# Optimization experiments

Measured on AMD Instinct MI355X. Metric: run time of the kernel, lower is better.

Reference implementation:

```python
import jax, jax.numpy as jnp
import numpy as np

C = 64           # channels
CPG = 8          # channel_per_group
G = C // CPG     # offset groups = 8
K = 27           # 3x3x3 taps
N, D, H, W = 2, 8, 56, 56


def conv3d(x, w, b=None):
    y = jax.lax.conv_general_dilated(
        x, w, window_strides=(1, 1, 1), padding=[(1, 1)] * 3,
        dimension_numbers=('NCDHW', 'OIDHW', 'NCDHW'))
    if b is not None:
        y = y + b.reshape(1, -1, 1, 1, 1)
    return y


def deform_conv3d(x, off, w, groups):
    # x: [N,C,D,H,W]; off: [N, G*3*27, D,H,W]; w: [O,C,3,3,3]
    n, cin, d, h, wd = x.shape
    cpg = cin // groups
    p = d * h * wd
    off = off.reshape(n, groups, K, 3, d, h, wd)
    # kernel tap displacements in (kd,kh,kw) order, each in {-1,0,1}
    r = jnp.arange(3, dtype=x.dtype) - 1.0
    taps = jnp.stack(jnp.meshgrid(r, r, r, indexing='ij'), axis=-1).reshape(K, 3)
    gd = jnp.arange(d, dtype=x.dtype)[:, None, None]
    gh = jnp.arange(h, dtype=x.dtype)[None, :, None]
    gw = jnp.arange(wd, dtype=x.dtype)[None, None, :]
    # sampling positions [N,G,K,D,H,W]
    pd = gd + taps[:, 0][:, None, None, None] + off[:, :, :, 0]
    ph = gh + taps[:, 1][:, None, None, None] + off[:, :, :, 1]
    pw = gw + taps[:, 2][:, None, None, None] + off[:, :, :, 2]
    d0 = jnp.floor(pd); h0 = jnp.floor(ph); w0 = jnp.floor(pw)
    fd, fh, fw = pd - d0, ph - h0, pw - w0
    d0 = d0.astype(jnp.int32); h0 = h0.astype(jnp.int32); w0 = w0.astype(jnp.int32)
    xflat = x.reshape(n, groups, cpg, p)[:, :, None]  # [N,G,1,Cpg,P]
    acc = jnp.zeros((n, groups, K, cpg, p), x.dtype)
    for cd in (0, 1):
        for ch in (0, 1):
            for cw in (0, 1):
                idd, idh, idw = d0 + cd, h0 + ch, w0 + cw
                wgt = ((fd if cd else 1.0 - fd)
                       * (fh if ch else 1.0 - fh)
                       * (fw if cw else 1.0 - fw))
                valid = ((idd >= 0) & (idd < d) & (idh >= 0) & (idh < h)
                         & (idw >= 0) & (idw < wd)).astype(x.dtype)
                lin = ((jnp.clip(idd, 0, d - 1) * h + jnp.clip(idh, 0, h - 1)) * wd
                       + jnp.clip(idw, 0, wd - 1))
                g = jnp.take_along_axis(xflat, lin.reshape(n, groups, K, 1, p), axis=-1)
                acc = acc + g * (wgt * valid).reshape(n, groups, K, 1, p)
    # [N,G,K,Cpg,P] -> [N,K,C,P]
    vals = acc.transpose(0, 2, 1, 3, 4).reshape(n, K, cin, p)
    out = jnp.einsum('oik,nkip->nop', w.reshape(w.shape[0], cin, K), vals)
    return out.reshape(n, -1, d, h, wd)


def batchnorm(x, gamma, beta, eps=1e-5):
    m = x.mean((0, 2, 3, 4), keepdims=True)
    v = x.var((0, 2, 3, 4), keepdims=True)
    return (gamma.reshape(1, -1, 1, 1, 1) * (x - m) * jax.lax.rsqrt(v + eps)
            + beta.reshape(1, -1, 1, 1, 1))


def setup_inputs() -> dict:
    key = jax.random.key(0)
    ks = jax.random.split(key, 4)
    fan = C * K
    x = jax.random.normal(ks[0], (N, C, D, H, W), jnp.float32)
    w_off = jax.random.normal(ks[1], (G * 3 * K, C, 3, 3, 3), jnp.float32) * 0.01
    b_off = jnp.zeros((G * 3 * K,), jnp.float32)
    w1 = jax.random.normal(ks[2], (C, C, 3, 3, 3), jnp.float32) / np.sqrt(fan).astype(np.float32)
    w2 = jax.random.normal(ks[3], (C, C, 3, 3, 3), jnp.float32) / np.sqrt(fan).astype(np.float32)
    return dict(x=x, w_off=w_off, b_off=b_off, w1=w1,
                gamma1=jnp.ones((C,), jnp.float32), beta1=jnp.zeros((C,), jnp.float32),
                w2=w2, b2=jnp.zeros((C,), jnp.float32),
                gamma2=jnp.ones((C,), jnp.float32), beta2=jnp.zeros((C,), jnp.float32))


def reference(x, w_off, b_off, w1, gamma1, beta1, w2, b2, gamma2, beta2):
    residual = x
    off = conv3d(x, w_off, b_off)
    out = deform_conv3d(x, off, w1, G)
    out = jax.nn.relu(batchnorm(out, gamma1, beta1))
    out = conv3d(out, w2, b2)
    out = batchnorm(out, gamma2, beta2) + residual
    return jax.nn.relu(out)
```

## Files before the change

kernel.cpp:

```cpp
#include <hip/hip_runtime.h>
#include <hip/hip_bf16.h>

#define N_ 2
#define C_ 64
#define D_ 8
#define H_ 56
#define W_ 56
#define HW_ (H_*W_)
#define P_ (D_*HW_)
#define G_ 8
#define CPG_ 8
#define K_ 27
#define CO_OFF_ 648
#define MP_ 768
#define KK_ 1728
#define KB_ (KK_*2)

typedef __attribute__((ext_vector_type(8))) short shortx8;
typedef __attribute__((ext_vector_type(4))) float floatx4;
#define AS1 __attribute__((address_space(1)))
#define AS3 __attribute__((address_space(3)))

__device__ inline float b2f(unsigned short u) {
    union { unsigned u; float f; } x; x.u = ((unsigned)u) << 16; return x.f;
}
__device__ inline unsigned short f2b(float f) {
    union { float f; unsigned u; } x; x.f = f;
    unsigned r = (x.u + 0x7fffu + ((x.u >> 16) & 1u)) >> 16;
    return (unsigned short)r;
}
__device__ inline float lof(unsigned u) { union { unsigned u; float f; } x; x.u = u << 16; return x.f; }
__device__ inline float hif(unsigned u) { union { unsigned u; float f; } x; x.u = u & 0xffff0000u; return x.f; }
__device__ inline unsigned cvt_pk_bf16(float a, float b) {
    unsigned r;
    asm("v_cvt_pk_bf16_f32 %0, %1, %2" : "=v"(r) : "v"(a), "v"(b));
    return r;
}


__global__ __launch_bounds__(256) void prep_kernel(
    const float* __restrict__ x,      unsigned short* __restrict__ xt,
    const float* __restrict__ w_off,  unsigned short* __restrict__ A1k,
    const float* __restrict__ w1,     unsigned short* __restrict__ A1t,
    const float* __restrict__ w2,     unsigned short* __restrict__ A2t)
{
    __shared__ unsigned short tile[64][65];
    int b   = blockIdx.x;
    int tid = threadIdx.x;

    if (b < 784) {
        int n  = b / (P_/64);
        int p0 = (b % (P_/64))*64;
        int j  = tid & 63;
        int c0 = (tid >> 6)*16;
        for (int r = 0; r < 16; ++r)
            tile[c0 + r][j] = f2b(x[((size_t)n*C_ + c0 + r)*P_ + p0 + j]);
        __syncthreads();
        unsigned* dst = (unsigned*)(xt + ((size_t)n*P_ + p0)*C_);
        #pragma unroll
        for (int it = 0; it < 8; ++it) {
            int wi  = it*256 + tid;
            int row = wi >> 5;
            int c   = (wi & 31)*2;
            unsigned lo = tile[c][row], hi = tile[c+1][row];
            dst[(size_t)row*32 + (wi & 31)] = lo | (hi << 16);
        }
    } else if (b < 784 + 5184) {
        int i = (b - 784)*256 + tid;
        int m = i / KK_, r = i % KK_;
        int kk = r / 64, ci = r % 64;
        A1k[i] = (m < CO_OFF_) ? f2b(w_off[((size_t)m*C_ + ci)*K_ + kk]) : (unsigned short)0;
    } else if (b < 784 + 5184 + 432) {
        int i = (b - 784 - 5184)*256 + tid;
        int o = i / KK_, r = i % KK_;
        int k = r / 64, ii = r % 64;
        A1t[i] = f2b(w1[((size_t)o*C_ + ii)*K_ + k]);
    } else {
        int i = (b - 784 - 5184 - 432)*256 + tid;
        int o = i / KK_, r = i % KK_;
        int k = r / 64, ii = r % 64;
        A2t[i] = f2b(w2[((size_t)o*C_ + ii)*K_ + k]);
    }
}

__global__ __launch_bounds__(256, 2) void conv_off_fused(
    const unsigned short* __restrict__ A,
    const unsigned short* __restrict__ xt,
    const float* __restrict__ bias,
    unsigned short* __restrict__ off2)
{
    __shared__ __align__(16) short SH[35840];
    int tid = threadIdx.x;
    int w = tid >> 6, lane = tid & 63;
    int lm = lane & 15, lq = lane >> 4;

    if (blockIdx.x < 2*490) {
        short* As0 = SH;
        short* Bs  = SH + 2*16*512;
        int n   = blockIdx.x / 490;
        int bid = blockIdx.x % 490;
        int mt = bid / 98, nt = bid % 98;
        int m0 = mt*128, p0 = nt*256;

        const unsigned short* xtn = xt + (size_t)n*P_*C_;
        unsigned short* out2 = off2 + (size_t)n*216*P_*3;

        const char* Ab0 = (const char*)A + (size_t)(m0 + w*32 + lm)*KB_ + lq*16;
        const char* Ab1 = Ab0 + (size_t)16*KB_;

        int oct = lane & 7;
        int prj[8], dj[8], hj[8], wj[8];
        #pragma unroll
        for (int j = 0; j < 8; ++j) {
            int prow = j*32 + w*8 + (lane >> 3);
            prj[j] = prow;
            int p = p0 + prow;
            dj[j] = p / HW_;
            int hw2 = p % HW_;
            hj[j] = hw2 / W_;
            wj[j] = hw2 % W_;
        }

        auto stageA = [&](int kt, int buf) {
            __builtin_amdgcn_global_load_lds((const AS1 unsigned*)(Ab0 + kt*128),      (AS3 unsigned*)(As0 + buf*8192 + (w*2)*512),     16, 0, 0);
            __builtin_amdgcn_global_load_lds((const AS1 unsigned*)(Ab1 + kt*128),      (AS3 unsigned*)(As0 + buf*8192 + (w*2+1)*512),   16, 0, 0);
            __builtin_amdgcn_global_load_lds((const AS1 unsigned*)(Ab0 + kt*128 + 64), (AS3 unsigned*)(As0 + buf*8192 + (8+w*2)*512),   16, 0, 0);
            __builtin_amdgcn_global_load_lds((const AS1 unsigned*)(Ab1 + kt*128 + 64), (AS3 unsigned*)(As0 + buf*8192 + (8+w*2+1)*512), 16, 0, 0);
        };
        auto loadB = [&](int kt, uint4* B) {
            int kd = kt/9 - 1, kh = (kt/3)%3 - 1, kw = kt%3 - 1;
            int delta = kd*HW_ + kh*W_ + kw;
            #pragma unroll
            for (int j = 0; j < 8; ++j) {
                bool v = ((unsigned)(dj[j]+kd) < (unsigned)D_) &&
                         ((unsigned)(hj[j]+kh) < (unsigned)H_) &&
                         ((unsigned)(wj[j]+kw) < (unsigned)W_);
                uint4 val = {0u,0u,0u,0u};
                if (v) val = *(const uint4*)(xtn + (size_t)(p0 + prj[j] + delta)*C_ + oct*8);
                B[j] = val;
            }
        };

        int mh = w >> 1, nh = w & 1;
        floatx4 acc[4][8];
        #pragma unroll
        for (int i = 0; i < 4; ++i)
            #pragma unroll
            for (int j = 0; j < 8; ++j)
                acc[i][j] = (floatx4){0.f, 0.f, 0.f, 0.f};

        uint4 Bcur[8], Bnext[8];
        #pragma unroll
        for (int j = 0; j < 8; ++j) Bnext[j] = (uint4){0u,0u,0u,0u};
        stageA(0, 0);
        loadB(0, Bcur);

        for (int kt = 0; kt < 27; ++kt) {
            int buf = kt & 1;
            __syncthreads();
            #pragma unroll
            for (int j = 0; j < 8; ++j) {
                int chunk = (oct>>2)*16 + (prj[j]>>4);
                *(uint4*)&Bs[chunk*512 + ((oct&3)*16 + ((prj[j]&15) ^ oct))*8] = Bcur[j];
            }
            __syncthreads();
            if (kt < 26) { stageA(kt+1, buf^1); loadB(kt+1, Bnext); }
            #pragma unroll
            for (int ks = 0; ks < 2; ++ks) {
                int swzB = (lq*16 + (lm ^ (ks*4 + lq)))*8;
                shortx8 a[4];
                #pragma unroll
                for (int i = 0; i < 4; ++i) a[i] = *(const shortx8*)&As0[buf*8192 + (ks*8 + 4*mh + i)*512 + lane*8];
                #pragma unroll
                for (int j = 0; j < 8; ++j) {
                    shortx8 b = *(const shortx8*)&Bs[(ks*16 + 8*nh + j)*512 + swzB];
                    #pragma unroll
                    for (int i = 0; i < 4; ++i)
                        acc[i][j] = __builtin_amdgcn_mfma_f32_16x16x32_bf16(a[i], b, acc[i][j], 0, 0, 0);
                }
            }
            #pragma unroll
            for (int j = 0; j < 8; ++j) Bcur[j] = Bnext[j];
        }

        #pragma unroll
        for (int i = 0; i < 4; ++i) {
            int cob = m0 + (4*mh+i)*16 + lq*4;
            #pragma unroll
            for (int r = 0; r < 4; ++r) {
                int co = cob + r;
                float bv = bias[co];
                int row2 = co / 3, comp = co % 3;
                size_t base = (size_t)row2*P_*3 + comp;
                #pragma unroll
                for (int j = 0; j < 8; ++j) {
                    int col = p0 + (8*nh+j)*16 + lm;
                    out2[base + (size_t)col*3] = f2b(acc[i][j][r] + bv);
                }
            }
        }
    } else {
        short* As = SH;
        short* Bs = SH + 54*512;
        int t  = blockIdx.x - 2*490;
        int n  = t / 196;
        int p0 = (t % 196)*128;

        const unsigned short* xtn = xt + (size_t)n*P_*C_;
        unsigned short* out2 = off2 + (size_t)n*216*P_*3;

        const char* Abase = (const char*)A + (size_t)(640 + lm)*KB_ + lq*16;
        for (int ch = w; ch < 54; ch += 4)
            __builtin_amdgcn_global_load_lds((const AS1 unsigned*)(Abase + ch*64),
                                             (AS3 unsigned*)(As + ch*512), 16, 0, 0);

        int oct = lane & 7;
        int prj[4], dj[4], hj[4], wj[4];
        #pragma unroll
        for (int j = 0; j < 4; ++j) {
            int prow = j*32 + w*8 + (lane >> 3);
            prj[j] = prow;
            int p = p0 + prow;
            dj[j] = p / HW_;
            int hw2 = p % HW_;
            hj[j] = hw2 / W_;
            wj[j] = hw2 % W_;
        }
        auto loadB = [&](int kt, uint4* B) {
            int kd = kt/9 - 1, kh = (kt/3)%3 - 1, kw = kt%3 - 1;
            int delta = kd*HW_ + kh*W_ + kw;
            #pragma unroll
            for (int j = 0; j < 4; ++j) {
                bool v = ((unsigned)(dj[j]+kd) < (unsigned)D_) &&
                         ((unsigned)(hj[j]+kh) < (unsigned)H_) &&
                         ((unsigned)(wj[j]+kw) < (unsigned)W_);
                uint4 val = {0u,0u,0u,0u};
                if (v) val = *(const uint4*)(xtn + (size_t)(p0 + prj[j] + delta)*C_ + oct*8);
                B[j] = val;
            }
        };

        floatx4 acc[2];
        acc[0] = (floatx4){0.f,0.f,0.f,0.f};
        acc[1] = (floatx4){0.f,0.f,0.f,0.f};

        uint4 Bcur[4], Bnext[4];
        #pragma unroll
        for (int j = 0; j < 4; ++j) Bnext[j] = (uint4){0u,0u,0u,0u};
        loadB(0, Bcur);

        for (int kt = 0; kt < 27; ++kt) {
            __syncthreads();
            #pragma unroll
            for (int j = 0; j < 4; ++j) {
                int chunk = (oct>>2)*8 + (prj[j]>>4);
                *(uint4*)&Bs[chunk*512 + ((oct&3)*16 + ((prj[j]&15) ^ oct))*8] = Bcur[j];
            }
            __syncthreads();
            if (kt < 26) loadB(kt+1, Bnext);
            #pragma unroll
            for (int ks = 0; ks < 2; ++ks) {
                int swzB = (lq*16 + (lm ^ (ks*4 + lq)))*8;
                shortx8 a = *(const shortx8*)&As[(kt*2 + ks)*512 + lane*8];
                #pragma unroll
                for (int j = 0; j < 2; ++j) {
                    shortx8 b = *(const shortx8*)&Bs[(ks*8 + w*2 + j)*512 + swzB];
                    acc[j] = __builtin_amdgcn_mfma_f32_16x16x32_bf16(a, b, acc[j], 0, 0, 0);
                }
            }
            #pragma unroll
            for (int j = 0; j < 4; ++j) Bcur[j] = Bnext[j];
        }

        #pragma unroll
        for (int j = 0; j < 2; ++j) {
            #pragma unroll
            for (int r = 0; r < 4; ++r) {
                int co = 640 + lq*4 + r;
                if (co < CO_OFF_) {
                    int col = p0 + w*32 + j*16 + lm;
                    out2[((size_t)(co/3)*P_ + col)*3 + (co%3)] = f2b(acc[j][r] + bias[co]);
                }
            }
        }
    }
}

__global__ __launch_bounds__(256) void deform_fused(
    const unsigned short* __restrict__ xt,
    const unsigned short* __restrict__ off2,
    const unsigned short* __restrict__ A,
    unsigned short* __restrict__ y1t,
    float* __restrict__ bn1p)
{
    __shared__ __align__(16) short SH[12288];
    int tid = threadIdx.x;
    int w = tid >> 6, lane = tid & 63;
    int n  = blockIdx.x / (P_/32);
    int p0 = (blockIdx.x % (P_/32))*32;
    int lm = lane & 15, lq = lane >> 4;

    const unsigned short* offn = off2 + (size_t)n*216*P_*3;
    const uint4* xg0 = (const uint4*)(xt + (size_t)n*P_*C_);

    const char* Ab = (const char*)A + (size_t)(w*16 + lm)*KB_ + lq*16;

    int g = lane & 7;
    int prow = tid >> 3;
    int p = p0 + prow;
    int dd = p / HW_;
    int hw2 = p % HW_;
    int hh = hw2 / W_;
    int ww = hw2 % W_;
    int bchunk = (g>>2)*2 + (prow>>4);
    int boffs  = ((g&3)*16 + ((prow&15) ^ g))*8;

    auto stageA = [&](int kt, int buf) {
        __builtin_amdgcn_global_load_lds((const AS1 unsigned*)(Ab + kt*128),      (AS3 unsigned*)(SH + buf*4096 + w*512),     16, 0, 0);
        __builtin_amdgcn_global_load_lds((const AS1 unsigned*)(Ab + kt*128 + 64), (AS3 unsigned*)(SH + buf*4096 + (4+w)*512), 16, 0, 0);
    };
    auto loadOff = [&](int kt, float* o) {
        size_t idx = ((size_t)(g*K_ + kt)*P_ + p)*3;
        o[0] = b2f(offn[idx]);
        o[1] = b2f(offn[idx + 1]);
        o[2] = b2f(offn[idx + 2]);
    };
    auto issueCorners = [&](int kt, float* o, uint4* V, float* Wt) {
        int kd = kt/9 - 1, kh = (kt/3)%3 - 1, kw = kt%3 - 1;
        float pd = (float)(dd + kd) + o[0];
        float ph = (float)(hh + kh) + o[1];
        float pw = (float)(ww + kw) + o[2];
        float fd0 = floorf(pd), fh0 = floorf(ph), fw0 = floorf(pw);
        int d0 = (int)fd0, h0 = (int)fh0, w0i = (int)fw0;
        float fd = pd - fd0, fh = ph - fh0, fw = pw - fw0;
        int dc0 = min(max(d0, 0), D_-1),   dc1 = min(max(d0+1, 0), D_-1);
        int hc0 = min(max(h0, 0), H_-1),   hc1 = min(max(h0+1, 0), H_-1);
        int wc0 = min(max(w0i, 0), W_-1),  wc1 = min(max(w0i+1, 0), W_-1);
        float wd0 = ((unsigned)d0      < (unsigned)D_) ? 1.f - fd : 0.f;
        float wd1 = ((unsigned)(d0+1)  < (unsigned)D_) ? fd       : 0.f;
        float wh0 = ((unsigned)h0      < (unsigned)H_) ? 1.f - fh : 0.f;
        float wh1 = ((unsigned)(h0+1)  < (unsigned)H_) ? fh       : 0.f;
        float ww0 = ((unsigned)w0i     < (unsigned)W_) ? 1.f - fw : 0.f;
        float ww1 = ((unsigned)(w0i+1) < (unsigned)W_) ? fw       : 0.f;
        int rb00 = (dc0*H_ + hc0)*W_, rb01 = (dc0*H_ + hc1)*W_;
        int rb10 = (dc1*H_ + hc0)*W_, rb11 = (dc1*H_ + hc1)*W_;
        float wdh00 = wd0*wh0, wdh01 = wd0*wh1, wdh10 = wd1*wh0, wdh11 = wd1*wh1;
        V[0] = xg0[(size_t)(rb00+wc0)*8 + g];  Wt[0] = wdh00*ww0;
        V[1] = xg0[(size_t)(rb00+wc1)*8 + g];  Wt[1] = wdh00*ww1;
        V[2] = xg0[(size_t)(rb01+wc0)*8 + g];  Wt[2] = wdh01*ww0;
        V[3] = xg0[(size_t)(rb01+wc1)*8 + g];  Wt[3] = wdh01*ww1;
        V[4] = xg0[(size_t)(rb10+wc0)*8 + g];  Wt[4] = wdh10*ww0;
        V[5] = xg0[(size_t)(rb10+wc1)*8 + g];  Wt[5] = wdh10*ww1;
        V[6] = xg0[(size_t)(rb11+wc0)*8 + g];  Wt[6] = wdh11*ww0;
        V[7] = xg0[(size_t)(rb11+wc1)*8 + g];  Wt[7] = wdh11*ww1;
    };
    auto reduceCorners = [&](uint4* V, float* Wt, uint4& o4) {
        float res[CPG_];
        #pragma unroll
        for (int c = 0; c < CPG_; ++c) res[c] = 0.f;
        #pragma unroll
        for (int c = 0; c < 8; ++c) {
            uint4 v4 = V[c];
            float wgt = Wt[c];
            res[0] = fmaf(wgt, lof(v4.x), res[0]);
            res[1] = fmaf(wgt, hif(v4.x), res[1]);
            res[2] = fmaf(wgt, lof(v4.y), res[2]);
            res[3] = fmaf(wgt, hif(v4.y), res[3]);
            res[4] = fmaf(wgt, lof(v4.z), res[4]);
            res[5] = fmaf(wgt, hif(v4.z), res[5]);
            res[6] = fmaf(wgt, lof(v4.w), res[6]);
            res[7] = fmaf(wgt, hif(v4.w), res[7]);
        }
        o4.x = cvt_pk_bf16(res[0], res[1]);
        o4.y = cvt_pk_bf16(res[2], res[3]);
        o4.z = cvt_pk_bf16(res[4], res[5]);
        o4.w = cvt_pk_bf16(res[6], res[7]);
    };

    int mh = w >> 1, nh = w & 1;
    floatx4 acc[2];
    acc[0] = (floatx4){0.f,0.f,0.f,0.f};
    acc[1] = (floatx4){0.f,0.f,0.f,0.f};

    float offA[3], offB[3], offT[3];
    uint4 Vv[8]; float Wt[8];
    uint4 o4cur;

    stageA(0, 0);
    loadOff(0, offA);
    loadOff(1, offB);
    issueCorners(0, offA, Vv, Wt);
    reduceCorners(Vv, Wt, o4cur);
    *(uint4*)&SH[8192 + bchunk*512 + boffs] = o4cur;

    for (int kt = 0; kt < 27; ++kt) {
        int buf = kt & 1;
        __syncthreads();
        if (kt < 26) {
            stageA(kt+1, buf^1);
            if (kt < 25) loadOff(kt+2, offT);
            issueCorners(kt+1, offB, Vv, Wt);
        }
        #pragma unroll
        for (int ks = 0; ks < 2; ++ks) {
            int swzB = (lq*16 + (lm ^ (ks*4 + lq)))*8;
            shortx8 b = *(const shortx8*)&SH[8192 + buf*2048 + (ks*2 + nh)*512 + swzB];
            #pragma unroll
            for (int i = 0; i < 2; ++i) {
                shortx8 a = *(const shortx8*)&SH[buf*4096 + (ks*4 + 2*mh+i)*512 + lane*8];
                acc[i] = __builtin_amdgcn_mfma_f32_16x16x32_bf16(a, b, acc[i], 0, 0, 0);
            }
        }
        if (kt < 26) {
            reduceCorners(Vv, Wt, o4cur);
            *(uint4*)&SH[8192 + (buf^1)*2048 + bchunk*512 + boffs] = o4cur;
            offB[0] = offT[0]; offB[1] = offT[1]; offB[2] = offT[2];
        }
    }

    __syncthreads();
    #pragma unroll
    for (int i = 0; i < 2; ++i) {
        int ob = mh*32 + i*16 + lq*4;
        int pc = nh*16 + lm;
        #pragma unroll
        for (int rr = 0; rr < 4; ++rr)
            SH[pc*72 + ob + rr] = (short)f2b(acc[i][rr]);
    }
    __syncthreads();
    {
        int row = tid >> 3, seg = tid & 7;
        uint4 v = *(const uint4*)&SH[row*72 + seg*8];
        *(uint4*)(y1t + ((size_t)n*P_ + p0 + row)*C_ + seg*8) = v;
    }
    {
        float* FS = (float*)(SH + 2560);
        float* FQ = FS + 256;
        int o = tid & 63, qt = tid >> 6;
        float s = 0.f, q = 0.f;
        #pragma unroll
        for (int pp = 0; pp < 8; ++pp) {
            float v = b2f((unsigned short)SH[(qt*8 + pp)*72 + o]);
            s += v;
            q = fmaf(v, v, q);
        }
        FS[qt*64 + o] = s;
        FQ[qt*64 + o] = q;
        __syncthreads();
        if (tid < 64) {
            float S = FS[tid] + FS[64+tid] + FS[128+tid] + FS[192+tid];
            float Q = FQ[tid] + FQ[64+tid] + FQ[128+tid] + FQ[192+tid];
            bn1p[(size_t)blockIdx.x*128 + tid]      = S;
            bn1p[(size_t)blockIdx.x*128 + 64 + tid] = Q;
        }
    }
}

__global__ __launch_bounds__(256) void conv2_fused(
    const unsigned short* __restrict__ y1t,
    const float* __restrict__ st1,
    const unsigned short* __restrict__ A,
    const float* __restrict__ bias,
    unsigned short* __restrict__ y2,
    float* __restrict__ part2)
{
    __shared__ __align__(16) short As[4][4096];
    __shared__ float sc[64], sf[64];
    __shared__ float SP[4][64], SQ[4][64];
    int tid = threadIdx.x;
    if (tid < 64) sc[tid] = st1[tid];
    else if (tid < 128) sf[tid-64] = st1[tid];
    int w = tid >> 6, lane = tid & 63;
    int n  = blockIdx.x / (P_/128);
    int p0 = (blockIdx.x % (P_/128))*128;
    int lm = lane & 15, lq = lane >> 4;

    const unsigned short* y1n = y1t + (size_t)n*P_*C_;
    unsigned short* y2n = y2 + (size_t)n*C_*P_;
    const char* Ab = (const char*)A + (size_t)(w*16 + lm)*KB_ + lq*16;

    int pj[2], dd[2], hh[2], ww[2];
    #pragma unroll
    for (int j = 0; j < 2; ++j) {
        pj[j] = p0 + j*64 + w*16 + lm;
        dd[j] = pj[j] / HW_;
        int hw2 = pj[j] % HW_;
        hh[j] = hw2 / W_;
        ww[j] = hw2 % W_;
    }

    auto stageA = [&](int kt) {
        int buf = kt & 3;
        __builtin_amdgcn_global_load_lds((const AS1 unsigned*)(Ab + kt*128),      (AS3 unsigned*)(&As[buf][w*512]),     16, 0, 0);
        __builtin_amdgcn_global_load_lds((const AS1 unsigned*)(Ab + kt*128 + 64), (AS3 unsigned*)(&As[buf][(4+w)*512]), 16, 0, 0);
    };
    auto issueV = [&](int kt, uint4 (*V)[2], int* M) {
        int kd = kt/9 - 1, kh = (kt/3)%3 - 1, kw = kt%3 - 1;
        int delta = kd*HW_ + kh*W_ + kw;
        #pragma unroll
        for (int j = 0; j < 2; ++j) {
            bool v = ((unsigned)(dd[j]+kd) < (unsigned)D_) &&
                     ((unsigned)(hh[j]+kh) < (unsigned)H_) &&
                     ((unsigned)(ww[j]+kw) < (unsigned)W_);
            M[j] = v ? 1 : 0;
            #pragma unroll
            for (int ks = 0; ks < 2; ++ks) {
                uint4 val = {0u,0u,0u,0u};
                if (v) val = *(const uint4*)(y1n + (size_t)(pj[j] + delta)*C_ + (ks*4 + lq)*8);
                V[j][ks] = val;
            }
        }
    };
    auto reduceT = [&](uint4 V, int ks, int M) -> shortx8 {
        uint4 o4 = {0u,0u,0u,0u};
        if (M) {
            int cb = (ks*4 + lq)*8;
            float r0 = fmaxf(lof(V.x)*sc[cb+0] + sf[cb+0], 0.f);
            float r1 = fmaxf(hif(V.x)*sc[cb+1] + sf[cb+1], 0.f);
            float r2 = fmaxf(lof(V.y)*sc[cb+2] + sf[cb+2], 0.f);
            float r3 = fmaxf(hif(V.y)*sc[cb+3] + sf[cb+3], 0.f);
            float r4 = fmaxf(lof(V.z)*sc[cb+4] + sf[cb+4], 0.f);
            float r5 = fmaxf(hif(V.z)*sc[cb+5] + sf[cb+5], 0.f);
            float r6 = fmaxf(lof(V.w)*sc[cb+6] + sf[cb+6], 0.f);
            float r7 = fmaxf(hif(V.w)*sc[cb+7] + sf[cb+7], 0.f);
            o4.x = cvt_pk_bf16(r0, r1);
            o4.y = cvt_pk_bf16(r2, r3);
            o4.z = cvt_pk_bf16(r4, r5);
            o4.w = cvt_pk_bf16(r6, r7);
        }
        return *(shortx8*)&o4;
    };

    floatx4 acc[4][2];
    #pragma unroll
    for (int i = 0; i < 4; ++i)
        #pragma unroll
        for (int j = 0; j < 2; ++j)
            acc[i][j] = (floatx4){0.f,0.f,0.f,0.f};

    auto mfmaTap = [&](int kt, uint4 (*V)[2], const int* M) {
        int buf = kt & 3;
        #pragma unroll
        for (int j = 0; j < 2; ++j) {
            shortx8 b0 = reduceT(V[j][0], 0, M[j]);
            shortx8 b1 = reduceT(V[j][1], 1, M[j]);
            #pragma unroll
            for (int i = 0; i < 4; ++i) {
                shortx8 a = *(const shortx8*)&As[buf][(0*4 + i)*512 + lane*8];
                acc[i][j] = __builtin_amdgcn_mfma_f32_16x16x32_bf16(a, b0, acc[i][j], 0, 0, 0);
            }
            #pragma unroll
            for (int i = 0; i < 4; ++i) {
                shortx8 a = *(const shortx8*)&As[buf][(1*4 + i)*512 + lane*8];
                acc[i][j] = __builtin_amdgcn_mfma_f32_16x16x32_bf16(a, b1, acc[i][j], 0, 0, 0);
            }
        }
    };

    uint4 VA[2][2], VB[2][2];
    int MA[2], MB[2];
    stageA(0); stageA(1);
    issueV(0, VA, MA);
    issueV(1, VB, MB);

    for (int kt = 0; kt < 26; kt += 2) {
        __syncthreads();
        stageA(kt+2);
        if (kt+3 <= 26) stageA(kt+3);
        {
            uint4 Vc[2][2];
            #pragma unroll
            for (int j = 0; j < 2; ++j) { Vc[j][0] = VA[j][0]; Vc[j][1] = VA[j][1]; }
            int Mc[2] = {MA[0], MA[1]};
            issueV(kt+2, VA, MA);
            mfmaTap(kt, Vc, Mc);
        }
        {
            uint4 Vc[2][2];
            #pragma unroll
            for (int j = 0; j < 2; ++j) { Vc[j][0] = VB[j][0]; Vc[j][1] = VB[j][1]; }
            int Mc[2] = {MB[0], MB[1]};
            if (kt+3 <= 26) issueV(kt+3, VB, MB);
            mfmaTap(kt+1, Vc, Mc);
        }
    }
    __syncthreads();
    mfmaTap(26, VA, MA);

    #pragma unroll
    for (int i = 0; i < 4; ++i) {
        #pragma unroll
        for (int r = 0; r < 4; ++r) {
            int co = i*16 + lq*4 + r;
            float v0 = acc[i][0][r] + bias[co];
            float v1 = acc[i][1][r] + bias[co];
            y2n[(size_t)co*P_ + pj[0]] = f2b(v0);
            y2n[(size_t)co*P_ + pj[1]] = f2b(v1);
            float s = v0 + v1;
            float q = v0*v0 + v1*v1;
            #pragma unroll
            for (int m = 1; m < 16; m <<= 1) {
                s += __shfl_xor(s, m);
                q += __shfl_xor(q, m);
            }
            if (lm == 0) { SP[w][co] = s; SQ[w][co] = q; }
        }
    }
    __syncthreads();
    if (tid < 64) {
        float S = SP[0][tid] + SP[1][tid] + SP[2][tid] + SP[3][tid];
        float Q = SQ[0][tid] + SQ[1][tid] + SQ[2][tid] + SQ[3][tid];
        part2[(size_t)blockIdx.x*128 + tid]      = S;
        part2[(size_t)blockIdx.x*128 + 64 + tid] = Q;
    }
}

__global__ __launch_bounds__(256) void stats_final_kernel(
    const float* __restrict__ part,
    const float* __restrict__ gamma, const float* __restrict__ beta,
    float* __restrict__ st1)
{
    int tid = threadIdx.x;
    int c = tid & 63, seg = tid >> 6;
    float S = 0.f, Q = 0.f;
    for (int b = seg*392; b < seg*392 + 392; ++b) {
        S += part[(size_t)b*128 + c];
        Q += part[(size_t)b*128 + 64 + c];
    }
    __shared__ float ss[256], qq[256];
    ss[tid] = S; qq[tid] = Q;
    __syncthreads();
    if (tid < 64) {
        float St = ss[tid] + ss[64+tid] + ss[128+tid] + ss[192+tid];
        float Qt = qq[tid] + qq[64+tid] + qq[128+tid] + qq[192+tid];
        const float inv = 1.f / (float)(N_*P_);
        float m = St * inv;
        float var = Qt * inv - m*m;
        float scale = rsqrtf(var + 1e-5f) * gamma[tid];
        st1[tid]      = scale;
        st1[64 + tid] = beta[tid] - m*scale;
    }
}

__global__ __launch_bounds__(256) void bn2_final_kernel(
    const float* __restrict__ part2,
    const float* __restrict__ gamma, const float* __restrict__ beta,
    float* __restrict__ st2)
{
    int tid = threadIdx.x;
    int c = tid & 63, seg = tid >> 6;
    float S = 0.f, Q = 0.f;
    for (int b = seg*98; b < seg*98 + 98; ++b) {
        S += part2[(size_t)b*128 + c];
        Q += part2[(size_t)b*128 + 64 + c];
    }
    __shared__ float ss[256], qq[256];
    ss[tid] = S; qq[tid] = Q;
    __syncthreads();
    if (tid < 64) {
        float St = ss[tid] + ss[64+tid] + ss[128+tid] + ss[192+tid];
        float Qt = qq[tid] + qq[64+tid] + qq[128+tid] + qq[192+tid];
        const float inv = 1.f / (float)(N_*P_);
        float m = St * inv;
        float var = Qt * inv - m*m;
        float scale = rsqrtf(var + 1e-5f) * gamma[tid];
        st2[tid]      = scale;
        st2[64 + tid] = beta[tid] - m*scale;
    }
}

__global__ __launch_bounds__(256) void bn_add_relu_kernel(
    const unsigned short* __restrict__ y2, const float* __restrict__ x,
    const float* __restrict__ st2, float* __restrict__ out)
{
    size_t i4 = ((size_t)blockIdx.x*256 + threadIdx.x)*4;
    int c = (int)((i4 / P_) % C_);
    float scale = st2[c], shift = st2[64 + c];
    uint2 yv = *(const uint2*)(y2 + i4);
    float4 xv = *(const float4*)(x + i4);
    float4 o;
    o.x = fmaxf(fmaf(lof(yv.x), scale, shift) + xv.x, 0.f);
    o.y = fmaxf(fmaf(hif(yv.x), scale, shift) + xv.y, 0.f);
    o.z = fmaxf(fmaf(lof(yv.y), scale, shift) + xv.z, 0.f);
    o.w = fmaxf(fmaf(hif(yv.y), scale, shift) + xv.w, 0.f);
    *(float4*)(out + i4) = o;
}

extern "C" void kernel_launch(void* const* d_in, const int* in_sizes, int n_in,
                              void* d_out, int out_size, void* d_ws, size_t ws_size,
                              hipStream_t stream) {
    const float* x     = (const float*)d_in[0];
    const float* w_off = (const float*)d_in[1];
    const float* b_off = (const float*)d_in[2];
    const float* w1    = (const float*)d_in[3];
    const float* g1    = (const float*)d_in[4];
    const float* be1   = (const float*)d_in[5];
    const float* w2    = (const float*)d_in[6];
    const float* b2    = (const float*)d_in[7];
    const float* g2    = (const float*)d_in[8];
    const float* be2   = (const float*)d_in[9];
    float* out = (float*)d_out;

    float* st1  = (float*)d_ws;
    float* st2  = st1 + 128;
    float* bn1p = st2 + 128;
    unsigned short* off2 = (unsigned short*)(bn1p + 1568*128);
    unsigned short* xt  = off2 + (size_t)N_*216*P_*3;
    unsigned short* y1t = xt  + (size_t)N_*P_*C_;
    unsigned short* y2  = y1t + (size_t)N_*P_*C_;
    unsigned short* A1k = y2  + (size_t)N_*C_*P_;
    unsigned short* A1t = A1k + (size_t)MP_*KK_;
    unsigned short* A2t = A1t + (size_t)C_*KK_;
    float* part2 = (float*)off2;

    prep_kernel<<<784 + 5184 + 432 + 432, 256, 0, stream>>>(
        x, xt, w_off, A1k, w1, A1t, w2, A2t);

    conv_off_fused<<<2*490 + 2*196, 256, 0, stream>>>(A1k, xt, b_off, off2);

    deform_fused<<<N_*(P_/32), 256, 0, stream>>>(xt, off2, A1t, y1t, bn1p);

    stats_final_kernel<<<1, 256, 0, stream>>>(bn1p, g1, be1, st1);

    conv2_fused<<<N_*(P_/128), 256, 0, stream>>>(y1t, st1, A2t, b2, y2, part2);

    bn2_final_kernel<<<1, 256, 0, stream>>>(part2, g2, be2, st2);
    bn_add_relu_kernel<<<(N_*C_*P_)/1024, 256, 0, stream>>>(y2, x, st2, out);
}
```

Measured before the change: 452.7 us.

## Double deform_fused pixel tile to 64 per block to reuse weight tiles

Each deform_fused block now covers 64 output positions instead of 32. Every thread samples two pixels per tap and each wave issues four MFMAs per k-step, so every staged weight A tile is reused across twice as many columns. This halves the A-tile global loads per output and halves the number of BN partial rows, which the stats reduction loop bounds now reflect. In exchange, register pressure and LDS use rise and the grid shrinks to half as many blocks, which may lower occupancy and reduce latency hiding for the gather loads.

Result: no change. 450.2 us (median of 2 runs) (-0.6%).

```diff
diff --git a/kernel.cpp b/kernel.cpp
--- a/kernel.cpp
+++ b/kernel.cpp
@@ -293,43 +293,48 @@
     unsigned short* __restrict__ y1t,
     float* __restrict__ bn1p)
 {
-    __shared__ __align__(16) short SH[12288];
+    __shared__ __align__(16) short SH[16384];
     int tid = threadIdx.x;
     int w = tid >> 6, lane = tid & 63;
-    int n  = blockIdx.x / (P_/32);
-    int p0 = (blockIdx.x % (P_/32))*32;
+    int n  = blockIdx.x / (P_/64);
+    int p0 = (blockIdx.x % (P_/64))*64;
     int lm = lane & 15, lq = lane >> 4;
+    int mh = w >> 1, nh = w & 1;
 
     const unsigned short* offn = off2 + (size_t)n*216*P_*3;
     const uint4* xg0 = (const uint4*)(xt + (size_t)n*P_*C_);
-
     const char* Ab = (const char*)A + (size_t)(w*16 + lm)*KB_ + lq*16;
 
     int g = lane & 7;
     int prow = tid >> 3;
-    int p = p0 + prow;
-    int dd = p / HW_;
-    int hw2 = p % HW_;
-    int hh = hw2 / W_;
-    int ww = hw2 % W_;
-    int bchunk = (g>>2)*2 + (prow>>4);
-    int boffs  = ((g&3)*16 + ((prow&15) ^ g))*8;
+    int dd[2], hh[2], ww[2];
+    #pragma unroll
+    for (int j = 0; j < 2; ++j) {
+        int p = p0 + j*32 + prow;
+        dd[j] = p / HW_;
+        int hw2 = p % HW_;
+        hh[j] = hw2 / W_;
+        ww[j] = hw2 % W_;
+    }
+    int bch0  = (g>>2)*4 + (prow>>4);
+    int boffs = ((g&3)*16 + ((prow&15) ^ g))*8;
+
+    const unsigned short* offp = offn + ((size_t)(g*K_)*P_ + p0 + prow)*3;
 
     auto stageA = [&](int kt, int buf) {
         __builtin_amdgcn_global_load_lds((const AS1 unsigned*)(Ab + kt*128),      (AS3 unsigned*)(SH + buf*4096 + w*512),     16, 0, 0);
         __builtin_amdgcn_global_load_lds((const AS1 unsigned*)(Ab + kt*128 + 64), (AS3 unsigned*)(SH + buf*4096 + (4+w)*512), 16, 0, 0);
     };
-    auto loadOff = [&](int kt, float* o) {
-        size_t idx = ((size_t)(g*K_ + kt)*P_ + p)*3;
-        o[0] = b2f(offn[idx]);
-        o[1] = b2f(offn[idx + 1]);
-        o[2] = b2f(offn[idx + 2]);
+    auto loadOff = [&](int kt, float (*o)[3]) {
+        const unsigned short* q = offp + (unsigned)(kt*(P_*3));
+        o[0][0] = b2f(q[0]);  o[0][1] = b2f(q[1]);  o[0][2] = b2f(q[2]);
+        o[1][0] = b2f(q[96]); o[1][1] = b2f(q[97]); o[1][2] = b2f(q[98]);
     };
-    auto issueCorners = [&](int kt, float* o, uint4* V, float* Wt) {
+    auto issueCornersJ = [&](int kt, const float* o, int j, uint4* V, float* Wt) {
         int kd = kt/9 - 1, kh = (kt/3)%3 - 1, kw = kt%3 - 1;
-        float pd = (float)(dd + kd) + o[0];
-        float ph = (float)(hh + kh) + o[1];
-        float pw = (float)(ww + kw) + o[2];
+        float pd = (float)(dd[j] + kd) + o[0];
+        float ph = (float)(hh[j] + kh) + o[1];
+        float pw = (float)(ww[j] + kw) + o[2];
         float fd0 = floorf(pd), fh0 = floorf(ph), fw0 = floorf(pw);
         int d0 = (int)fd0, h0 = (int)fh0, w0i = (int)fw0;
         float fd = pd - fd0, fh = ph - fh0, fw = pw - fw0;
@@ -354,7 +359,7 @@
         V[6] = xg0[(size_t)(rb11+wc0)*8 + g];  Wt[6] = wdh11*ww0;
         V[7] = xg0[(size_t)(rb11+wc1)*8 + g];  Wt[7] = wdh11*ww1;
     };
-    auto reduceCorners = [&](uint4* V, float* Wt, uint4& o4) {
+    auto reduceCorners = [&](const uint4* V, const float* Wt, uint4& o4) {
         float res[CPG_];
         #pragma unroll
         for (int c = 0; c < CPG_; ++c) res[c] = 0.f;
@@ -377,21 +382,26 @@
         o4.w = cvt_pk_bf16(res[6], res[7]);
     };
 
-    int mh = w >> 1, nh = w & 1;
-    floatx4 acc[2];
-    acc[0] = (floatx4){0.f,0.f,0.f,0.f};
-    acc[1] = (floatx4){0.f,0.f,0.f,0.f};
-
-    float offA[3], offB[3], offT[3];
-    uint4 Vv[8]; float Wt[8];
+    floatx4 acc[2][2];
+    #pragma unroll
+    for (int i = 0; i < 2; ++i)
+        #pragma unroll
+        for (int j = 0; j < 2; ++j)
+            acc[i][j] = (floatx4){0.f,0.f,0.f,0.f};
+
+    float offA[2][3], offB[2][3], offT[2][3];
+    uint4 VA[2][8]; float WA[2][8];
     uint4 o4cur;
 
     stageA(0, 0);
     loadOff(0, offA);
     loadOff(1, offB);
-    issueCorners(0, offA, Vv, Wt);
-    reduceCorners(Vv, Wt, o4cur);
-    *(uint4*)&SH[8192 + bchunk*512 + boffs] = o4cur;
+    issueCornersJ(0, offA[0], 0, VA[0], WA[0]);
+    issueCornersJ(0, offA[1], 1, VA[1], WA[1]);
+    reduceCorners(VA[0], WA[0], o4cur);
+    *(uint4*)&SH[8192 + bch0*512 + boffs] = o4cur;
+    reduceCorners(VA[1], WA[1], o4cur);
+    *(uint4*)&SH[8192 + (bch0+2)*512 + boffs] = o4cur;
 
     for (int kt = 0; kt < 27; ++kt) {
         int buf = kt & 1;
@@ -399,48 +409,62 @@
         if (kt < 26) {
             stageA(kt+1, buf^1);
             if (kt < 25) loadOff(kt+2, offT);
-            issueCorners(kt+1, offB, Vv, Wt);
+            issueCornersJ(kt+1, offB[0], 0, VA[0], WA[0]);
+            issueCornersJ(kt+1, offB[1], 1, VA[1], WA[1]);
         }
         #pragma unroll
         for (int ks = 0; ks < 2; ++ks) {
             int swzB = (lq*16 + (lm ^ (ks*4 + lq)))*8;
-            shortx8 b = *(const shortx8*)&SH[8192 + buf*2048 + (ks*2 + nh)*512 + swzB];
-            #pragma unroll
-            for (int i = 0; i < 2; ++i) {
-                shortx8 a = *(const shortx8*)&SH[buf*4096 + (ks*4 + 2*mh+i)*512 + lane*8];
-                acc[i] = __builtin_amdgcn_mfma_f32_16x16x32_bf16(a, b, acc[i], 0, 0, 0);
+            #pragma unroll
+            for (int j2 = 0; j2 < 2; ++j2) {
+                shortx8 b = *(const shortx8*)&SH[8192 + buf*4096 + (ks*4 + nh*2 + j2)*512 + swzB];
+                #pragma unroll
+                for (int i = 0; i < 2; ++i) {
+                    shortx8 a = *(const shortx8*)&SH[buf*4096 + (ks*4 + 2*mh+i)*512 + lane*8];
+                    acc[i][j2] = __builtin_amdgcn_mfma_f32_16x16x32_bf16(a, b, acc[i][j2], 0, 0, 0);
+                }
             }
         }
         if (kt < 26) {
-            reduceCorners(Vv, Wt, o4cur);
-            *(uint4*)&SH[8192 + (buf^1)*2048 + bchunk*512 + boffs] = o4cur;
-            offB[0] = offT[0]; offB[1] = offT[1]; offB[2] = offT[2];
+            reduceCorners(VA[0], WA[0], o4cur);
+            *(uint4*)&SH[8192 + (buf^1)*4096 + bch0*512 + boffs] = o4cur;
+            reduceCorners(VA[1], WA[1], o4cur);
+            *(uint4*)&SH[8192 + (buf^1)*4096 + (bch0+2)*512 + boffs] = o4cur;
+            #pragma unroll
+            for (int j = 0; j < 2; ++j) {
+                offB[j][0] = offT[j][0]; offB[j][1] = offT[j][1]; offB[j][2] = offT[j][2];
+            }
         }
     }
 
     __syncthreads();
     #pragma unroll
     for (int i = 0; i < 2; ++i) {
-        int ob = mh*32 + i*16 + lq*4;
-        int pc = nh*16 + lm;
-        #pragma unroll
-        for (int rr = 0; rr < 4; ++rr)
-            SH[pc*72 + ob + rr] = (short)f2b(acc[i][rr]);
+        #pragma unroll
+        for (int j2 = 0; j2 < 2; ++j2) {
+            int ob = mh*32 + i*16 + lq*4;
+            int pc = nh*32 + j2*16 + lm;
+            #pragma unroll
+            for (int rr = 0; rr < 4; ++rr)
+                SH[pc*72 + ob + rr] = (short)f2b(acc[i][j2][rr]);
+        }
     }
     __syncthreads();
-    {
-        int row = tid >> 3, seg = tid & 7;
+    #pragma unroll
+    for (int it = 0; it < 2; ++it) {
+        int wi = it*256 + tid;
+        int row = wi >> 3, seg = wi & 7;
         uint4 v = *(const uint4*)&SH[row*72 + seg*8];
         *(uint4*)(y1t + ((size_t)n*P_ + p0 + row)*C_ + seg*8) = v;
     }
     {
-        float* FS = (float*)(SH + 2560);
+        float* FS = (float*)(SH + 10240);
         float* FQ = FS + 256;
         int o = tid & 63, qt = tid >> 6;
         float s = 0.f, q = 0.f;
         #pragma unroll
-        for (int pp = 0; pp < 8; ++pp) {
-            float v = b2f((unsigned short)SH[(qt*8 + pp)*72 + o]);
+        for (int pp = 0; pp < 16; ++pp) {
+            float v = b2f((unsigned short)SH[(qt*16 + pp)*72 + o]);
             s += v;
             q = fmaf(v, v, q);
         }
@@ -623,7 +647,7 @@
     int tid = threadIdx.x;
     int c = tid & 63, seg = tid >> 6;
     float S = 0.f, Q = 0.f;
-    for (int b = seg*392; b < seg*392 + 392; ++b) {
+    for (int b = seg*196; b < seg*196 + 196; ++b) {
         S += part[(size_t)b*128 + c];
         Q += part[(size_t)b*128 + 64 + c];
     }
@@ -718,7 +742,7 @@
 
     conv_off_fused<<<2*490 + 2*196, 256, 0, stream>>>(A1k, xt, b_off, off2);
 
-    deform_fused<<<N_*(P_/32), 256, 0, stream>>>(xt, off2, A1t, y1t, bn1p);
+    deform_fused<<<N_*(P_/64), 256, 0, stream>>>(xt, off2, A1t, y1t, bn1p);
 
     stats_final_kernel<<<1, 256, 0, stream>>>(bn1p, g1, be1, st1);
 
```
